# Optimization experiments

Hardware: AMD Instinct MI355X
Metric: run time of the kernel (lower is better)

Reference implementation:

```python
import jax, jax.numpy as jnp
import numpy as np

N_NODES = 200_000
N_EDGES = 6_400_000
N_GRAPHS = 2048
VOCAB = 10_000
EMB = 64
HID = 64
NUM_CLASSES = 2


def setup_inputs() -> dict:
    key = jax.random.key(0)
    ks = jax.random.split(key, 12)
    x = jax.random.randint(ks[0], (N_NODES,), 0, VOCAB)
    edge_index = jax.random.randint(ks[1], (2, N_EDGES), 0, N_NODES)
    batch = jnp.sort(jax.random.randint(ks[2], (N_NODES,), 0, N_GRAPHS))
    s = 0.05
    return {
        "x": x,
        "edge_index": edge_index,
        "batch": batch,
        "emb": jax.random.normal(ks[3], (VOCAB, EMB), jnp.float32) * s,
        "W1_l": jax.random.normal(ks[4], (HID, EMB), jnp.float32) * s,
        "b1": jnp.zeros((HID,), jnp.float32),
        "W1_r": jax.random.normal(ks[5], (HID, EMB), jnp.float32) * s,
        "W2_l": jax.random.normal(ks[6], (HID, HID), jnp.float32) * s,
        "b2": jnp.zeros((HID,), jnp.float32),
        "W2_r": jax.random.normal(ks[7], (HID, HID), jnp.float32) * s,
        "Wout": jax.random.normal(ks[8], (NUM_CLASSES, HID), jnp.float32) * s,
        "bout": jnp.zeros((NUM_CLASSES,), jnp.float32),
    }


def _sage_conv(h, src, dst, W_l, b, W_r):
    # mean-aggregate messages from src at dst (PyG SAGEConv, aggr='mean')
    msg_sum = jax.ops.segment_sum(h[src], dst, num_segments=N_NODES)
    cnt = jax.ops.segment_sum(jnp.ones((src.shape[0], 1), h.dtype), dst,
                              num_segments=N_NODES)
    mean = msg_sum / jnp.maximum(cnt, 1.0)  # zero-degree nodes -> 0
    # out = lin_l(mean_neighbors) + lin_r(x); lin_r has no bias in PyG
    return mean @ W_l.T + b + h @ W_r.T


def reference(x, edge_index, batch, emb, W1_l, b1, W1_r, W2_l, b2, W2_r,
              Wout, bout):
    src, dst = edge_index[0], edge_index[1]
    h = emb[x]  # [N, EMB]
    h = jax.nn.relu(_sage_conv(h, src, dst, W1_l, b1, W1_r))
    h = jax.nn.relu(_sage_conv(h, src, dst, W2_l, b2, W2_r))
    # global_mean_pool over graph ids
    pooled = jax.ops.segment_sum(h, batch, num_segments=N_GRAPHS)
    cnt = jax.ops.segment_sum(jnp.ones((h.shape[0], 1), h.dtype), batch,
                              num_segments=N_GRAPHS)
    pooled = pooled / jnp.maximum(cnt, 1.0)
    return pooled @ Wout.T + bout  # [N_GRAPHS, NUM_CLASSES]
```

## Files before the change

kernel.cpp:

```cpp
#include <hip/hip_runtime.h>
#include <hip/hip_fp16.h>
#include <stdint.h>


#define NPW 4
#define NPB 4
#define NBUCK 256
#define TILE 4096
#define EPT 16
#define MAXN 1024

__device__ __forceinline__ int bucket_of(int dstv, int n_nodes) {
  return (int)(((unsigned)dstv * 256u) / (unsigned)n_nodes);
}

__device__ __forceinline__ void acc8h(float* a, uint4 u, float m) {
  const __half2* hp = (const __half2*)&u;
#pragma unroll
  for (int q = 0; q < 4; ++q) {
    float2 f = __half22float2(hp[q]);
    a[2 * q]     = fmaf(m, f.x, a[2 * q]);
    a[2 * q + 1] = fmaf(m, f.y, a[2 * q + 1]);
  }
}

__device__ __forceinline__ void acctree(float* a, uint4 u0, uint4 u1, uint4 u2, uint4 u3) {
  const __half2* p0 = (const __half2*)&u0;
  const __half2* p1 = (const __half2*)&u1;
  const __half2* p2 = (const __half2*)&u2;
  const __half2* p3 = (const __half2*)&u3;
#pragma unroll
  for (int q = 0; q < 4; ++q) {
    __half2 s = __hadd2(__hadd2(p0[q], p1[q]), __hadd2(p2[q], p3[q]));
    float2 f = __half22float2(s);
    a[2 * q]     += f.x;
    a[2 * q + 1] += f.y;
  }
}

__global__ void k_init(int* __restrict__ gcur, int cap) {
  gcur[threadIdx.x] = threadIdx.x * cap;
}

__global__ void k_part(const int* __restrict__ src, const int* __restrict__ dst,
                       int* __restrict__ gcur, unsigned* __restrict__ pairs,
                       int n_edges, int n_nodes, int chunk) {
  __shared__ int hist[NBUCK];
  __shared__ int base[NBUCK];
  int t = threadIdx.x;
  int beg = blockIdx.x * chunk;
  int end = min(beg + chunk, n_edges);
  for (int tbeg = beg; tbeg < end; tbeg += TILE) {
    int cnt = min(TILE, end - tbeg);
    hist[t] = 0;
    __syncthreads();
    unsigned pk[EPT];
    int r[EPT], bk[EPT];
    bool v[EPT];
#pragma unroll
    for (int k = 0; k < EPT; ++k) {
      int li = k * 256 + t;
      v[k] = li < cnt;
      if (v[k]) {
        int i = tbeg + li;
        int s = src[i];
        int d = dst[i];
        bk[k] = bucket_of(d, n_nodes);
        unsigned nb0 = ((unsigned)bk[k] * (unsigned)n_nodes + 255u) >> 8;
        pk[k] = (((unsigned)d - nb0) << 18) | (unsigned)s;
        r[k] = atomicAdd(&hist[bk[k]], 1);
      }
    }
    __syncthreads();
    base[t] = (hist[t] > 0) ? atomicAdd(&gcur[t], hist[t]) : 0;
    __syncthreads();
#pragma unroll
    for (int k = 0; k < EPT; ++k)
      if (v[k]) pairs[base[bk[k]] + r[k]] = pk[k];
    __syncthreads();
  }
}

__global__ void k_bscan2(const int* __restrict__ gcur, int* __restrict__ bbase,
                         int cap, int n_edges) {
  __shared__ int s[NBUCK];
  int t = threadIdx.x;
  s[t] = gcur[t] - t * cap;
  __syncthreads();
  for (int off = 1; off < NBUCK; off <<= 1) {
    int add = (t >= off) ? s[t - off] : 0;
    __syncthreads();
    s[t] += add;
    __syncthreads();
  }
  bbase[t] = (t == 0) ? 0 : s[t - 1];
  if (t == NBUCK - 1) bbase[NBUCK] = n_edges;
}

__global__ void k_bucket(const unsigned* __restrict__ pairs, const int* __restrict__ gcur,
                         const int* __restrict__ bbase, const int* __restrict__ x,
                         int* __restrict__ offs, unsigned* __restrict__ idx,
                         int n_nodes, int n_edges, int cap) {
  __shared__ int lcnt[MAXN];
  __shared__ int lcur[MAXN];
  __shared__ int stmp[256];
  int b = blockIdx.x, t = threadIdx.x;
  int nb0 = (int)((((unsigned)b * (unsigned)n_nodes) + 255u) >> 8);
  int nb1 = (int)((((unsigned)(b + 1) * (unsigned)n_nodes) + 255u) >> 8);
  if (nb1 > n_nodes) nb1 = n_nodes;
  int nn = nb1 - nb0;
  int rbeg = b * cap;
  int rend = gcur[b];
  int obase = bbase[b];
  for (int i = t; i < nn; i += 256) lcnt[i] = 0;
  __syncthreads();
  for (int i = rbeg + t; i < rend; i += 256)
    atomicAdd(&lcnt[pairs[i] >> 18], 1);
  __syncthreads();
  int i0 = t * 4;
  int v0 = (i0 + 0 < nn) ? lcnt[i0 + 0] : 0;
  int v1 = (i0 + 1 < nn) ? lcnt[i0 + 1] : 0;
  int v2 = (i0 + 2 < nn) ? lcnt[i0 + 2] : 0;
  int v3 = (i0 + 3 < nn) ? lcnt[i0 + 3] : 0;
  stmp[t] = v0 + v1 + v2 + v3;
  __syncthreads();
  for (int off = 1; off < 256; off <<= 1) {
    int add = (t >= off) ? stmp[t - off] : 0;
    __syncthreads();
    stmp[t] += add;
    __syncthreads();
  }
  int run = obase + ((t == 0) ? 0 : stmp[t - 1]);
  if (i0 + 0 < nn) { lcur[i0 + 0] = run; offs[nb0 + i0 + 0] = run; run += v0; }
  if (i0 + 1 < nn) { lcur[i0 + 1] = run; offs[nb0 + i0 + 1] = run; run += v1; }
  if (i0 + 2 < nn) { lcur[i0 + 2] = run; offs[nb0 + i0 + 2] = run; run += v2; }
  if (i0 + 3 < nn) { lcur[i0 + 3] = run; offs[nb0 + i0 + 3] = run; run += v3; }
  if (b == NBUCK - 1 && t == 0) offs[n_nodes] = n_edges;
  __syncthreads();
  for (int i = rbeg + t; i < rend; i += 256) {
    unsigned e = pairs[i];
    int s = (int)(e & 0x3FFFFu);
    int pos = atomicAdd(&lcur[e >> 18], 1);
    idx[pos] = ((unsigned)x[s] << 18) | (unsigned)s;
  }
}

__global__ void k_transpose4(const float* __restrict__ a0, const float* __restrict__ a1,
                             const float* __restrict__ a2, const float* __restrict__ a3,
                             float* __restrict__ wt) {
  const float* s = (blockIdx.x == 0) ? a0 : (blockIdx.x == 1) ? a1 : (blockIdx.x == 2) ? a2 : a3;
  float* d = wt + blockIdx.x * 4096;
  for (int i = threadIdx.x; i < 4096; i += blockDim.x) {
    int r = i >> 6, c = i & 63;
    d[c * 64 + r] = s[i];
  }
}

__global__ void k_prep(const float* __restrict__ emb, const float* __restrict__ w1lT,
                       const float* __restrict__ w1rT, const float* __restrict__ b1,
                       __half* __restrict__ te, float* __restrict__ trb, int vocab) {
  __shared__ float se[NPB][64];
  int wid = threadIdx.x >> 6, lane = threadIdx.x & 63;
  int v = blockIdx.x * NPB + wid;
  if (v >= vocab) return;
  se[wid][lane] = emb[(size_t)v * 64 + lane];
  __syncwarp();
  float aL = 0.f, aR = b1[lane];
#pragma unroll 8
  for (int f = 0; f < 64; ++f) {
    float ev = se[wid][f];
    aL = fmaf(ev, w1lT[f * 64 + lane], aL);
    aR = fmaf(ev, w1rT[f * 64 + lane], aR);
  }
  te[(size_t)v * 64 + lane] = __float2half(aL);
  trb[(size_t)v * 64 + lane] = aR;
}

__global__ __launch_bounds__(64) void
k_conv1(const unsigned* __restrict__ idx, const int* __restrict__ offs,
        const __half* __restrict__ te, const float* __restrict__ trb,
        const int* __restrict__ x, const float* __restrict__ w2lT,
        const float* __restrict__ w2rT, const float* __restrict__ b2,
        __half* __restrict__ g1, float* __restrict__ s1, int n_nodes) {
  __shared__ float sm[NPW][64];
  int lane = threadIdx.x;
  int r8 = lane >> 3, s8 = (lane & 7) << 3;
  int nbase = blockIdx.x * NPW;
  if (nbase >= n_nodes) return;
  int nvalid = min(NPW, n_nodes - nbase);

  for (int i = 0; i < nvalid; ++i) {
    int node = nbase + i;
    int beg = offs[node], end = offs[node + 1];
    float a[8];
#pragma unroll
    for (int q = 0; q < 8; ++q) a[q] = 0.f;
    for (int c = beg; c < end; c += 64) {
      int nit = min(end - c, 64);
      unsigned eidx = idx[c + min(lane, nit - 1)];
      int nfull = nit & ~31;
      for (int k = 0; k < nfull; k += 32) {
        int k0 = k + r8;
        int v0 = (int)(__shfl(eidx, k0) >> 18);
        int v1 = (int)(__shfl(eidx, k0 + 8) >> 18);
        int v2 = (int)(__shfl(eidx, k0 + 16) >> 18);
        int v3 = (int)(__shfl(eidx, k0 + 24) >> 18);
        uint4 u0 = *(const uint4*)(te + ((size_t)v0 << 6) + s8);
        uint4 u1 = *(const uint4*)(te + ((size_t)v1 << 6) + s8);
        uint4 u2 = *(const uint4*)(te + ((size_t)v2 << 6) + s8);
        uint4 u3 = *(const uint4*)(te + ((size_t)v3 << 6) + s8);
        acctree(a, u0, u1, u2, u3);
      }
      if (nit & 31) {
        int k0 = nfull + r8, k1 = k0 + 8, k2 = k0 + 16, k3 = k0 + 24;
        int v0 = (int)(__shfl(eidx, min(k0, nit - 1)) >> 18);
        int v1 = (int)(__shfl(eidx, min(k1, nit - 1)) >> 18);
        int v2 = (int)(__shfl(eidx, min(k2, nit - 1)) >> 18);
        int v3 = (int)(__shfl(eidx, min(k3, nit - 1)) >> 18);
        uint4 u0 = *(const uint4*)(te + ((size_t)v0 << 6) + s8);
        uint4 u1 = *(const uint4*)(te + ((size_t)v1 << 6) + s8);
        uint4 u2 = *(const uint4*)(te + ((size_t)v2 << 6) + s8);
        uint4 u3 = *(const uint4*)(te + ((size_t)v3 << 6) + s8);
        acc8h(a, u0, (k0 < nit) ? 1.f : 0.f);
        acc8h(a, u1, (k1 < nit) ? 1.f : 0.f);
        acc8h(a, u2, (k2 < nit) ? 1.f : 0.f);
        acc8h(a, u3, (k3 < nit) ? 1.f : 0.f);
      }
    }
#pragma unroll
    for (int q = 0; q < 8; ++q) {
      a[q] += __shfl_xor(a[q], 8);
      a[q] += __shfl_xor(a[q], 16);
      a[q] += __shfl_xor(a[q], 32);
    }
    int deg = end - beg;
    float inv = (deg > 0) ? 1.f / (float)deg : 0.f;
    if (lane < 8) {
      const float* tp = trb + ((size_t)x[node] << 6) + s8;
      float4 t0 = *(const float4*)tp;
      float4 t1 = *(const float4*)(tp + 4);
      float4 h0, h1;
      h0.x = fmaxf(fmaf(a[0], inv, t0.x), 0.f);
      h0.y = fmaxf(fmaf(a[1], inv, t0.y), 0.f);
      h0.z = fmaxf(fmaf(a[2], inv, t0.z), 0.f);
      h0.w = fmaxf(fmaf(a[3], inv, t0.w), 0.f);
      h1.x = fmaxf(fmaf(a[4], inv, t1.x), 0.f);
      h1.y = fmaxf(fmaf(a[5], inv, t1.y), 0.f);
      h1.z = fmaxf(fmaf(a[6], inv, t1.z), 0.f);
      h1.w = fmaxf(fmaf(a[7], inv, t1.w), 0.f);
      *(float4*)&sm[i][s8] = h0;
      *(float4*)&sm[i][s8 + 4] = h1;
    }
  }
  __syncthreads();

  float b2v = b2[lane];
  float aL[NPW], aR[NPW];
#pragma unroll
  for (int i = 0; i < NPW; ++i) { aL[i] = 0.f; aR[i] = b2v; }
  const float* smw = &sm[0][0];
#pragma unroll 8
  for (int f = 0; f < 64; ++f) {
    float wl = w2lT[f * 64 + lane];
    float wr = w2rT[f * 64 + lane];
#pragma unroll
    for (int i = 0; i < NPW; ++i) {
      float h = smw[i * 64 + f];
      aL[i] = fmaf(h, wl, aL[i]);
      aR[i] = fmaf(h, wr, aR[i]);
    }
  }
  for (int i = 0; i < nvalid; ++i) {
    int node = nbase + i;
    g1[((size_t)node << 6) + lane] = __float2half(aL[i]);
    s1[((size_t)node << 6) + lane] = aR[i];
  }
}

__global__ __launch_bounds__(64) void
k_conv2(const unsigned* __restrict__ idx, const int* __restrict__ offs,
        const __half* __restrict__ g1, const float* __restrict__ s1,
        const float* __restrict__ wout, float* __restrict__ o, int n_nodes) {
  __shared__ float sm[64];
  int lane = threadIdx.x;
  int r8 = lane >> 3, s8 = (lane & 7) << 3;
  int node = blockIdx.x;
  if (node >= n_nodes) return;
  int beg = offs[node], end = offs[node + 1];
  float a[8];
#pragma unroll
  for (int q = 0; q < 8; ++q) a[q] = 0.f;
  for (int c = beg; c < end; c += 64) {
    int nit = min(end - c, 64);
    unsigned eidx = idx[c + min(lane, nit - 1)];
    int nfull = nit & ~31;
    for (int k = 0; k < nfull; k += 32) {
      int k0 = k + r8;
      int v0 = (int)(__shfl(eidx, k0) & 0x3FFFFu);
      int v1 = (int)(__shfl(eidx, k0 + 8) & 0x3FFFFu);
      int v2 = (int)(__shfl(eidx, k0 + 16) & 0x3FFFFu);
      int v3 = (int)(__shfl(eidx, k0 + 24) & 0x3FFFFu);
      uint4 u0 = *(const uint4*)(g1 + ((size_t)v0 << 6) + s8);
      uint4 u1 = *(const uint4*)(g1 + ((size_t)v1 << 6) + s8);
      uint4 u2 = *(const uint4*)(g1 + ((size_t)v2 << 6) + s8);
      uint4 u3 = *(const uint4*)(g1 + ((size_t)v3 << 6) + s8);
      acctree(a, u0, u1, u2, u3);
    }
    if (nit & 31) {
      int k0 = nfull + r8, k1 = k0 + 8, k2 = k0 + 16, k3 = k0 + 24;
      int v0 = (int)(__shfl(eidx, min(k0, nit - 1)) & 0x3FFFFu);
      int v1 = (int)(__shfl(eidx, min(k1, nit - 1)) & 0x3FFFFu);
      int v2 = (int)(__shfl(eidx, min(k2, nit - 1)) & 0x3FFFFu);
      int v3 = (int)(__shfl(eidx, min(k3, nit - 1)) & 0x3FFFFu);
      uint4 u0 = *(const uint4*)(g1 + ((size_t)v0 << 6) + s8);
      uint4 u1 = *(const uint4*)(g1 + ((size_t)v1 << 6) + s8);
      uint4 u2 = *(const uint4*)(g1 + ((size_t)v2 << 6) + s8);
      uint4 u3 = *(const uint4*)(g1 + ((size_t)v3 << 6) + s8);
      acc8h(a, u0, (k0 < nit) ? 1.f : 0.f);
      acc8h(a, u1, (k1 < nit) ? 1.f : 0.f);
      acc8h(a, u2, (k2 < nit) ? 1.f : 0.f);
      acc8h(a, u3, (k3 < nit) ? 1.f : 0.f);
    }
  }
#pragma unroll
  for (int q = 0; q < 8; ++q) {
    a[q] += __shfl_xor(a[q], 8);
    a[q] += __shfl_xor(a[q], 16);
    a[q] += __shfl_xor(a[q], 32);
  }
  int deg = end - beg;
  float inv = (deg > 0) ? 1.f / (float)deg : 0.f;
  if (lane < 8) {
#pragma unroll
    for (int q = 0; q < 8; ++q) sm[s8 + q] = a[q] * inv;
  }
  __syncthreads();
  float h2 = fmaxf(sm[lane] + s1[((size_t)node << 6) + lane], 0.f);
  float p0 = h2 * wout[lane];
  float p1 = h2 * wout[64 + lane];
  for (int off = 32; off > 0; off >>= 1) {
    p0 += __shfl_down(p0, off);
    p1 += __shfl_down(p1, off);
  }
  if (lane == 0) {
    o[((size_t)node << 1) + 0] = p0;
    o[((size_t)node << 1) + 1] = p1;
  }
}

__global__ void k_goffs(const int* __restrict__ batch, int* __restrict__ goffs,
                        int n_nodes, int n_graphs) {
  int i = blockIdx.x * blockDim.x + threadIdx.x;
  if (i >= n_nodes) return;
  int b = batch[i];
  int bp = (i == 0) ? -1 : batch[i - 1];
  for (int g = bp + 1; g <= b; ++g) goffs[g] = i;
  if (i == n_nodes - 1)
    for (int g = b + 1; g <= n_graphs; ++g) goffs[g] = n_nodes;
}

__global__ void k_pool(const float2* __restrict__ o, const int* __restrict__ goffs,
                       const float* __restrict__ bout, float* __restrict__ out,
                       int n_graphs) {
  int wid = threadIdx.x >> 6, lane = threadIdx.x & 63;
  int g = blockIdx.x * NPB + wid;
  if (g >= n_graphs) return;
  int beg = goffs[g], end = goffs[g + 1];
  float a0 = 0.f, a1 = 0.f;
  for (int n = beg + lane; n < end; n += 64) {
    float2 v = o[n];
    a0 += v.x;
    a1 += v.y;
  }
  for (int off = 32; off > 0; off >>= 1) {
    a0 += __shfl_down(a0, off);
    a1 += __shfl_down(a1, off);
  }
  if (lane == 0) {
    int cnt = end - beg;
    float inv = (cnt > 0) ? 1.f / (float)cnt : 0.f;
    out[g * 2 + 0] = a0 * inv + bout[0];
    out[g * 2 + 1] = a1 * inv + bout[1];
  }
}

extern "C" void kernel_launch(void* const* d_in, const int* in_sizes, int n_in,
                              void* d_out, int out_size, void* d_ws, size_t ws_size,
                              hipStream_t stream) {
  const int* x = (const int*)d_in[0];
  const int* ei = (const int*)d_in[1];
  const int* batch = (const int*)d_in[2];
  const float* emb = (const float*)d_in[3];
  const float* W1l = (const float*)d_in[4];
  const float* b1 = (const float*)d_in[5];
  const float* W1r = (const float*)d_in[6];
  const float* W2l = (const float*)d_in[7];
  const float* b2 = (const float*)d_in[8];
  const float* W2r = (const float*)d_in[9];
  const float* Wout = (const float*)d_in[10];
  const float* bout = (const float*)d_in[11];
  float* out = (float*)d_out;

  int n_nodes = in_sizes[0];
  int n_edges = in_sizes[1] / 2;
  int vocab = in_sizes[3] / 64;
  int n_graphs = out_size / 2;
  const int* src = ei;
  const int* dst = ei + n_edges;

  int cap = n_edges / NBUCK + n_edges / (NBUCK * 8) + 1024;

  char* p = (char*)d_ws;
  auto alloc = [&](size_t bytes) -> void* {
    void* r = (void*)p;
    p += (bytes + 255) & ~(size_t)255;
    return r;
  };
  __half* te = (__half*)alloc((size_t)vocab * 64 * 2);
  float* trb = (float*)alloc((size_t)vocab * 64 * 4);
  float* wt = (float*)alloc(4 * 4096 * 4);
  int* offs = (int*)alloc((size_t)(n_nodes + 1) * 4);
  int* goffs = (int*)alloc((size_t)(n_graphs + 1) * 4);
  int* bbase = (int*)alloc((NBUCK + 1) * 4);
  int* gcur = (int*)alloc(NBUCK * 4);
  unsigned* idx = (unsigned*)alloc((size_t)n_edges * 4);
  size_t pairs_bytes = (size_t)NBUCK * cap * 4;
  size_t g1_bytes = (size_t)n_nodes * 64 * 2;
  unsigned* pairs = (unsigned*)alloc(pairs_bytes > g1_bytes ? pairs_bytes : g1_bytes);
  float* s1 = (float*)alloc((size_t)n_nodes * 64 * 4);
  float* o = (float*)alloc((size_t)n_nodes * 2 * 4);
  __half* g1 = (__half*)pairs;

  k_init<<<1, NBUCK, 0, stream>>>(gcur, cap);
  k_transpose4<<<4, 256, 0, stream>>>(W1l, W1r, W2l, W2r, wt);
  k_prep<<<(vocab + NPB - 1) / NPB, 64 * NPB, 0, stream>>>(emb, wt, wt + 4096, b1, te, trb, vocab);

  int part_blocks = 512;
  int chunk = (n_edges + part_blocks - 1) / part_blocks;
  k_part<<<part_blocks, 256, 0, stream>>>(src, dst, gcur, pairs, n_edges, n_nodes, chunk);
  k_bscan2<<<1, NBUCK, 0, stream>>>(gcur, bbase, cap, n_edges);
  k_bucket<<<NBUCK, 256, 0, stream>>>(pairs, gcur, bbase, x, offs, idx, n_nodes, n_edges, cap);

  k_goffs<<<(n_nodes + 255) / 256, 256, 0, stream>>>(batch, goffs, n_nodes, n_graphs);

  k_conv1<<<(n_nodes + NPW - 1) / NPW, 64, 0, stream>>>(idx, offs, te, trb, x, wt + 8192, wt + 12288, b2, g1, s1, n_nodes);
  k_conv2<<<n_nodes, 64, 0, stream>>>(idx, offs, g1, s1, Wout, o, n_nodes);
  k_pool<<<(n_graphs + NPB - 1) / NPB, 64 * NPB, 0, stream>>>((const float2*)o, goffs, bout, out, n_graphs);
}
```

Baseline: 436.0 us.

## Split conv1 into per-node gather and MFMA fp16 GEMM for layer-2 projections

The fused conv1 kernel, which gathered neighbours for four nodes per block and then did a scalar fp32 64x64 projection, is split in two. The first kernel gathers one node per block and writes the layer-1 activations as fp16. The second packs W2l/W2r into an MFMA B layout and computes both projections for 16-node tiles with 16x16x32 fp16 MFMA instructions. This trades an extra fp16 round trip of h1 through memory and one more launch for much cheaper projection arithmetic and more parallel gather blocks. The h1 input to the GEMM is now fp16, where it was fp32 before.

New measurement: 405.2 us. 7.1% less time.

```diff
diff --git a/kernel.cpp b/kernel.cpp
--- a/kernel.cpp
+++ b/kernel.cpp
@@ -9,6 +9,9 @@
 #define TILE 4096
 #define EPT 16
 #define MAXN 1024
+
+typedef __attribute__((ext_vector_type(8))) _Float16 half8;
+typedef __attribute__((ext_vector_type(4))) float f32x4;
 
 __device__ __forceinline__ int bucket_of(int dstv, int n_nodes) {
   return (int)(((unsigned)dstv * 256u) / (unsigned)n_nodes);
@@ -156,6 +159,17 @@
   }
 }
 
+__global__ void k_packB(const float* __restrict__ W2l, const float* __restrict__ W2r,
+                        __half* __restrict__ pB) {
+  int i = blockIdx.x * 256 + threadIdx.x;
+  if (i >= 8192) return;
+  int j = i & 7, l = (i >> 3) & 63, kt = (i >> 9) & 1, nt = (i >> 10) & 3, mat = i >> 12;
+  int k = kt * 32 + (l >> 4) * 8 + j;
+  int n = nt * 16 + (l & 15);
+  const float* W = mat ? W2r : W2l;
+  pB[i] = __float2half(W[n * 64 + k]);
+}
+
 __global__ void k_prep(const float* __restrict__ emb, const float* __restrict__ w1lT,
                        const float* __restrict__ w1rT, const float* __restrict__ b1,
                        __half* __restrict__ te, float* __restrict__ trb, int vocab) {
@@ -177,103 +191,105 @@
 }
 
 __global__ __launch_bounds__(64) void
-k_conv1(const unsigned* __restrict__ idx, const int* __restrict__ offs,
-        const __half* __restrict__ te, const float* __restrict__ trb,
-        const int* __restrict__ x, const float* __restrict__ w2lT,
-        const float* __restrict__ w2rT, const float* __restrict__ b2,
-        __half* __restrict__ g1, float* __restrict__ s1, int n_nodes) {
-  __shared__ float sm[NPW][64];
+k_gather1(const unsigned* __restrict__ idx, const int* __restrict__ offs,
+          const __half* __restrict__ te, const float* __restrict__ trb,
+          const int* __restrict__ x, __half* __restrict__ h1, int n_nodes) {
   int lane = threadIdx.x;
   int r8 = lane >> 3, s8 = (lane & 7) << 3;
-  int nbase = blockIdx.x * NPW;
-  if (nbase >= n_nodes) return;
-  int nvalid = min(NPW, n_nodes - nbase);
-
-  for (int i = 0; i < nvalid; ++i) {
-    int node = nbase + i;
-    int beg = offs[node], end = offs[node + 1];
-    float a[8];
-#pragma unroll
-    for (int q = 0; q < 8; ++q) a[q] = 0.f;
-    for (int c = beg; c < end; c += 64) {
-      int nit = min(end - c, 64);
-      unsigned eidx = idx[c + min(lane, nit - 1)];
-      int nfull = nit & ~31;
-      for (int k = 0; k < nfull; k += 32) {
-        int k0 = k + r8;
-        int v0 = (int)(__shfl(eidx, k0) >> 18);
-        int v1 = (int)(__shfl(eidx, k0 + 8) >> 18);
-        int v2 = (int)(__shfl(eidx, k0 + 16) >> 18);
-        int v3 = (int)(__shfl(eidx, k0 + 24) >> 18);
-        uint4 u0 = *(const uint4*)(te + ((size_t)v0 << 6) + s8);
-        uint4 u1 = *(const uint4*)(te + ((size_t)v1 << 6) + s8);
-        uint4 u2 = *(const uint4*)(te + ((size_t)v2 << 6) + s8);
-        uint4 u3 = *(const uint4*)(te + ((size_t)v3 << 6) + s8);
-        acctree(a, u0, u1, u2, u3);
+  int node = blockIdx.x;
+  if (node >= n_nodes) return;
+  int beg = offs[node], end = offs[node + 1];
+  float a[8];
+#pragma unroll
+  for (int q = 0; q < 8; ++q) a[q] = 0.f;
+  for (int c = beg; c < end; c += 64) {
+    int nit = min(end - c, 64);
+    unsigned eidx = idx[c + min(lane, nit - 1)];
+    int nfull = nit & ~31;
+    for (int k = 0; k < nfull; k += 32) {
+      int k0 = k + r8;
+      int v0 = (int)(__shfl(eidx, k0) >> 18);
+      int v1 = (int)(__shfl(eidx, k0 + 8) >> 18);
+      int v2 = (int)(__shfl(eidx, k0 + 16) >> 18);
+      int v3 = (int)(__shfl(eidx, k0 + 24) >> 18);
+      uint4 u0 = *(const uint4*)(te + ((size_t)v0 << 6) + s8);
+      uint4 u1 = *(const uint4*)(te + ((size_t)v1 << 6) + s8);
+      uint4 u2 = *(const uint4*)(te + ((size_t)v2 << 6) + s8);
+      uint4 u3 = *(const uint4*)(te + ((size_t)v3 << 6) + s8);
+      acctree(a, u0, u1, u2, u3);
+    }
+    if (nit & 31) {
+      int k0 = nfull + r8, k1 = k0 + 8, k2 = k0 + 16, k3 = k0 + 24;
+      int v0 = (int)(__shfl(eidx, min(k0, nit - 1)) >> 18);
+      int v1 = (int)(__shfl(eidx, min(k1, nit - 1)) >> 18);
+      int v2 = (int)(__shfl(eidx, min(k2, nit - 1)) >> 18);
+      int v3 = (int)(__shfl(eidx, min(k3, nit - 1)) >> 18);
+      uint4 u0 = *(const uint4*)(te + ((size_t)v0 << 6) + s8);
+      uint4 u1 = *(const uint4*)(te + ((size_t)v1 << 6) + s8);
+      uint4 u2 = *(const uint4*)(te + ((size_t)v2 << 6) + s8);
+      uint4 u3 = *(const uint4*)(te + ((size_t)v3 << 6) + s8);
+      acc8h(a, u0, (k0 < nit) ? 1.f : 0.f);
+      acc8h(a, u1, (k1 < nit) ? 1.f : 0.f);
+      acc8h(a, u2, (k2 < nit) ? 1.f : 0.f);
+      acc8h(a, u3, (k3 < nit) ? 1.f : 0.f);
+    }
+  }
+#pragma unroll
+  for (int q = 0; q < 8; ++q) {
+    a[q] += __shfl_xor(a[q], 8);
+    a[q] += __shfl_xor(a[q], 16);
+    a[q] += __shfl_xor(a[q], 32);
+  }
+  int deg = end - beg;
+  float inv = (deg > 0) ? 1.f / (float)deg : 0.f;
+  if (lane < 8) {
+    const float* tp = trb + ((size_t)x[node] << 6) + s8;
+    float4 t0 = *(const float4*)tp;
+    float4 t1 = *(const float4*)(tp + 4);
+    __half hh[8];
+    hh[0] = __float2half(fmaxf(fmaf(a[0], inv, t0.x), 0.f));
+    hh[1] = __float2half(fmaxf(fmaf(a[1], inv, t0.y), 0.f));
+    hh[2] = __float2half(fmaxf(fmaf(a[2], inv, t0.z), 0.f));
+    hh[3] = __float2half(fmaxf(fmaf(a[3], inv, t0.w), 0.f));
+    hh[4] = __float2half(fmaxf(fmaf(a[4], inv, t1.x), 0.f));
+    hh[5] = __float2half(fmaxf(fmaf(a[5], inv, t1.y), 0.f));
+    hh[6] = __float2half(fmaxf(fmaf(a[6], inv, t1.z), 0.f));
+    hh[7] = __float2half(fmaxf(fmaf(a[7], inv, t1.w), 0.f));
+    *(uint4*)(h1 + ((size_t)node << 6) + s8) = *(uint4*)hh;
+  }
+}
+
+__global__ __launch_bounds__(64) void
+k_gemm(const __half* __restrict__ h1, const __half* __restrict__ pB,
+       const float* __restrict__ b2, __half* __restrict__ g1,
+       float* __restrict__ s1, int n_nodes) {
+  int lane = threadIdx.x;
+  int nbase = blockIdx.x * 16;
+  int row = lane & 15, grp = lane >> 4;
+  const half8 a0 = *(const half8*)(h1 + ((size_t)(nbase + row) << 6) + grp * 8);
+  const half8 a1 = *(const half8*)(h1 + ((size_t)(nbase + row) << 6) + 32 + grp * 8);
+#pragma unroll
+  for (int t = 0; t < 8; ++t) {
+    const half8 b0 = *(const half8*)(pB + (t * 2 + 0) * 512 + lane * 8);
+    const half8 b1 = *(const half8*)(pB + (t * 2 + 1) * 512 + lane * 8);
+    f32x4 acc = {0.f, 0.f, 0.f, 0.f};
+    acc = __builtin_amdgcn_mfma_f32_16x16x32_f16(a0, b0, acc, 0, 0, 0);
+    acc = __builtin_amdgcn_mfma_f32_16x16x32_f16(a1, b1, acc, 0, 0, 0);
+    int out = (t & 3) * 16 + (lane & 15);
+    if (t < 4) {
+#pragma unroll
+      for (int r = 0; r < 4; ++r) {
+        int node = nbase + grp * 4 + r;
+        if (node < n_nodes) g1[((size_t)node << 6) + out] = __float2half(acc[r]);
       }
-      if (nit & 31) {
-        int k0 = nfull + r8, k1 = k0 + 8, k2 = k0 + 16, k3 = k0 + 24;
-        int v0 = (int)(__shfl(eidx, min(k0, nit - 1)) >> 18);
-        int v1 = (int)(__shfl(eidx, min(k1, nit - 1)) >> 18);
-        int v2 = (int)(__shfl(eidx, min(k2, nit - 1)) >> 18);
-        int v3 = (int)(__shfl(eidx, min(k3, nit - 1)) >> 18);
-        uint4 u0 = *(const uint4*)(te + ((size_t)v0 << 6) + s8);
-        uint4 u1 = *(const uint4*)(te + ((size_t)v1 << 6) + s8);
-        uint4 u2 = *(const uint4*)(te + ((size_t)v2 << 6) + s8);
-        uint4 u3 = *(const uint4*)(te + ((size_t)v3 << 6) + s8);
-        acc8h(a, u0, (k0 < nit) ? 1.f : 0.f);
-        acc8h(a, u1, (k1 < nit) ? 1.f : 0.f);
-        acc8h(a, u2, (k2 < nit) ? 1.f : 0.f);
-        acc8h(a, u3, (k3 < nit) ? 1.f : 0.f);
+    } else {
+      float bias = b2[out];
+#pragma unroll
+      for (int r = 0; r < 4; ++r) {
+        int node = nbase + grp * 4 + r;
+        if (node < n_nodes) s1[((size_t)node << 6) + out] = acc[r] + bias;
       }
     }
-#pragma unroll
-    for (int q = 0; q < 8; ++q) {
-      a[q] += __shfl_xor(a[q], 8);
-      a[q] += __shfl_xor(a[q], 16);
-      a[q] += __shfl_xor(a[q], 32);
-    }
-    int deg = end - beg;
-    float inv = (deg > 0) ? 1.f / (float)deg : 0.f;
-    if (lane < 8) {
-      const float* tp = trb + ((size_t)x[node] << 6) + s8;
-      float4 t0 = *(const float4*)tp;
-      float4 t1 = *(const float4*)(tp + 4);
-      float4 h0, h1;
-      h0.x = fmaxf(fmaf(a[0], inv, t0.x), 0.f);
-      h0.y = fmaxf(fmaf(a[1], inv, t0.y), 0.f);
-      h0.z = fmaxf(fmaf(a[2], inv, t0.z), 0.f);
-      h0.w = fmaxf(fmaf(a[3], inv, t0.w), 0.f);
-      h1.x = fmaxf(fmaf(a[4], inv, t1.x), 0.f);
-      h1.y = fmaxf(fmaf(a[5], inv, t1.y), 0.f);
-      h1.z = fmaxf(fmaf(a[6], inv, t1.z), 0.f);
-      h1.w = fmaxf(fmaf(a[7], inv, t1.w), 0.f);
-      *(float4*)&sm[i][s8] = h0;
-      *(float4*)&sm[i][s8 + 4] = h1;
-    }
-  }
-  __syncthreads();
-
-  float b2v = b2[lane];
-  float aL[NPW], aR[NPW];
-#pragma unroll
-  for (int i = 0; i < NPW; ++i) { aL[i] = 0.f; aR[i] = b2v; }
-  const float* smw = &sm[0][0];
-#pragma unroll 8
-  for (int f = 0; f < 64; ++f) {
-    float wl = w2lT[f * 64 + lane];
-    float wr = w2rT[f * 64 + lane];
-#pragma unroll
-    for (int i = 0; i < NPW; ++i) {
-      float h = smw[i * 64 + f];
-      aL[i] = fmaf(h, wl, aL[i]);
-      aR[i] = fmaf(h, wr, aR[i]);
-    }
-  }
-  for (int i = 0; i < nvalid; ++i) {
-    int node = nbase + i;
-    g1[((size_t)node << 6) + lane] = __float2half(aL[i]);
-    s1[((size_t)node << 6) + lane] = aR[i];
   }
 }
 
@@ -409,6 +425,7 @@
   const int* dst = ei + n_edges;
 
   int cap = n_edges / NBUCK + n_edges / (NBUCK * 8) + 1024;
+  int ntiles = (n_nodes + 15) / 16;
 
   char* p = (char*)d_ws;
   auto alloc = [&](size_t bytes) -> void* {
@@ -418,12 +435,14 @@
   };
   __half* te = (__half*)alloc((size_t)vocab * 64 * 2);
   float* trb = (float*)alloc((size_t)vocab * 64 * 4);
-  float* wt = (float*)alloc(4 * 4096 * 4);
+  float* wt = (float*)alloc(2 * 4096 * 4);
+  __half* pB = (__half*)alloc(8192 * 2);
   int* offs = (int*)alloc((size_t)(n_nodes + 1) * 4);
   int* goffs = (int*)alloc((size_t)(n_graphs + 1) * 4);
   int* bbase = (int*)alloc((NBUCK + 1) * 4);
   int* gcur = (int*)alloc(NBUCK * 4);
   unsigned* idx = (unsigned*)alloc((size_t)n_edges * 4);
+  __half* h1 = (__half*)alloc((size_t)(ntiles * 16) * 64 * 2);
   size_t pairs_bytes = (size_t)NBUCK * cap * 4;
   size_t g1_bytes = (size_t)n_nodes * 64 * 2;
   unsigned* pairs = (unsigned*)alloc(pairs_bytes > g1_bytes ? pairs_bytes : g1_bytes);
@@ -432,8 +451,9 @@
   __half* g1 = (__half*)pairs;
 
   k_init<<<1, NBUCK, 0, stream>>>(gcur, cap);
-  k_transpose4<<<4, 256, 0, stream>>>(W1l, W1r, W2l, W2r, wt);
+  k_transpose4<<<2, 256, 0, stream>>>(W1l, W1r, W1l, W1l, wt);
   k_prep<<<(vocab + NPB - 1) / NPB, 64 * NPB, 0, stream>>>(emb, wt, wt + 4096, b1, te, trb, vocab);
+  k_packB<<<32, 256, 0, stream>>>(W2l, W2r, pB);
 
   int part_blocks = 512;
   int chunk = (n_edges + part_blocks - 1) / part_blocks;
@@ -443,7 +463,8 @@
 
   k_goffs<<<(n_nodes + 255) / 256, 256, 0, stream>>>(batch, goffs, n_nodes, n_graphs);
 
-  k_conv1<<<(n_nodes + NPW - 1) / NPW, 64, 0, stream>>>(idx, offs, te, trb, x, wt + 8192, wt + 12288, b2, g1, s1, n_nodes);
+  k_gather1<<<n_nodes, 64, 0, stream>>>(idx, offs, te, trb, x, h1, n_nodes);
+  k_gemm<<<ntiles, 64, 0, stream>>>(h1, pB, b2, g1, s1, n_nodes);
   k_conv2<<<n_nodes, 64, 0, stream>>>(idx, offs, g1, s1, Wout, o, n_nodes);
   k_pool<<<(n_graphs + NPB - 1) / NPB, 64 * NPB, 0, stream>>>((const float2*)o, goffs, bout, out, n_graphs);
 }
```
